# Kernel optimization log

Measured on AMD Instinct MI355X. Metric: run time of the kernel, lower is better.

Reference implementation:

```python
import jax, jax.numpy as jnp
import numpy as np

N, E, F_IN, H, C = 50000, 800000, 128, 4, 73
HC = H * C  # 292
NEG_SLOPE_ATT = 0.2   # GATv2 attention leaky relu
NEG_SLOPE_ACT = 0.01  # F.leaky_relu default
BN_EPS = 1e-5


def setup_inputs() -> dict:
    key = jax.random.key(0)
    ks = jax.random.split(key, 20)
    rn = lambda k, shp, s=0.05: (jax.random.normal(k, shp, jnp.float32) * s)
    inp = {
        'x': jax.random.normal(ks[0], (N, F_IN), jnp.float32),
        'edge_index': jax.random.randint(ks[1], (2, E), 0, N, jnp.int64),
        # conv1 (in=F_IN)
        'Wl1': rn(ks[2], (HC, F_IN)), 'bl1': rn(ks[3], (HC,)),
        'Wr1': rn(ks[4], (HC, F_IN)), 'br1': rn(ks[5], (HC,)),
        'att1': rn(ks[6], (H, C)), 'b1': rn(ks[7], (HC,)),
        # conv2 (in=HC)
        'Wl2': rn(ks[8], (HC, HC)), 'bl2': rn(ks[9], (HC,)),
        'Wr2': rn(ks[10], (HC, HC)), 'br2': rn(ks[11], (HC,)),
        'att2': rn(ks[12], (H, C)), 'b2': rn(ks[13], (HC,)),
        # shared BatchNorm1d(HC)
        'gamma': jnp.ones((HC,), jnp.float32), 'beta': jnp.zeros((HC,), jnp.float32),
        # classifier Linear(HC, 2)
        'Wc': rn(ks[14], (2, HC)), 'bc': rn(ks[15], (2,)),
    }
    return inp


def _gatv2(x, src, dst, Wl, bl, Wr, br, att, b):
    # lin_l on source, lin_r on target (PyG GATv2Conv, share_weights=False)
    xl = (x @ Wl.T + bl).reshape(-1, H, C)  # [N,H,C]
    xr = (x @ Wr.T + br).reshape(-1, H, C)
    f = xl[src] + xr[dst]                    # [E,H,C] edge-wise gather
    s = jnp.einsum('ehc,hc->eh', jax.nn.leaky_relu(f, NEG_SLOPE_ATT), att)
    # segment softmax over incoming edges of each destination node
    m = jax.ops.segment_max(s, dst, num_segments=N)
    ex = jnp.exp(s - m[dst])
    den = jax.ops.segment_sum(ex, dst, num_segments=N)
    alpha = ex / (den[dst] + 1e-16)          # [E,H]
    out = jax.ops.segment_sum(alpha[:, :, None] * xl[src], dst, num_segments=N)
    return out.reshape(-1, HC) + b           # concat heads + bias


def _bn(x, gamma, beta):
    mu = jnp.mean(x, axis=0)
    var = jnp.mean((x - mu) ** 2, axis=0)
    return (x - mu) * jax.lax.rsqrt(var + BN_EPS) * gamma + beta


def reference(x, edge_index, Wl1, bl1, Wr1, br1, att1, b1,
              Wl2, bl2, Wr2, br2, att2, b2, gamma, beta, Wc, bc):
    src, dst = edge_index[0], edge_index[1]
    h = _gatv2(x, src, dst, Wl1, bl1, Wr1, br1, att1, b1)
    h = jax.nn.leaky_relu(_bn(h, gamma, beta), NEG_SLOPE_ACT)
    h = _gatv2(h, src, dst, Wl2, bl2, Wr2, br2, att2, b2)
    h = jax.nn.leaky_relu(_bn(h, gamma, beta), NEG_SLOPE_ACT)
    return h @ Wc.T + bc
```

## Files before the change

### kernel.cpp

```cpp
#include <hip/hip_runtime.h>

#define HCDIM 292
#define NHEAD 4
#define CDIM 73
#define SLOTS 5
#define NPERM 320
#define BN_EPS 1e-5f

using u16x8 = __attribute__((ext_vector_type(8))) unsigned short;
using s16x8 = __attribute__((ext_vector_type(8))) short;
using f32x4 = __attribute__((ext_vector_type(4))) float;
using u16x4 = __attribute__((ext_vector_type(4))) unsigned short;

__device__ inline ushort f2bf(float f) {
  unsigned int u = __float_as_uint(f);
  u += 0x7FFFu + ((u >> 16) & 1u);
  return (ushort)(u >> 16);
}
__device__ inline float bf2f(ushort v) {
  return __uint_as_float(((unsigned int)v) << 16);
}

__device__ inline int perm2feat(int p, bool& valid) {
  int h, c;
  if (p < 256) {
    h = p >> 6;
    c = ((p & 3) << 4) | ((p >> 2) & 15);
    valid = true;
  } else {
    int q = p - 256;
    h = q >> 4;
    c = 64 + (q & 15);
    valid = (q & 15) < (CDIM - 64);
  }
  return h * CDIM + c;
}

__global__ void k_zero_i32(int* __restrict__ p, int n) {
  int i = blockIdx.x * blockDim.x + threadIdx.x;
  if (i < n) p[i] = 0;
}
__global__ void k_zero_f32(float* __restrict__ p, int n) {
  int i = blockIdx.x * blockDim.x + threadIdx.x;
  if (i < n) p[i] = 0.f;
}

__global__ void k_wperm(const float* __restrict__ W, const float* __restrict__ b,
                        ushort* __restrict__ Wp, float* __restrict__ pb,
                        int Kin, int Kpad, int kperm) {
  int p = blockIdx.x, t = threadIdx.x;
  bool pv;
  int gn = perm2feat(p, pv);
  int gk = t;
  bool kv = t < Kin;
  if (kperm) { bool v2; gk = perm2feat(t, v2); kv = v2; }
  ushort v = 0;
  if (pv && kv) v = f2bf(W[(size_t)gn * Kin + gk]);
  Wp[(size_t)p * Kpad + t] = v;
  if (t == 0) pb[p] = pv ? b[gn] : 0.f;
}

__global__ void k_vecperm(const float* __restrict__ att1, const float* __restrict__ b1,
                          const float* __restrict__ att2, const float* __restrict__ b2,
                          const float* __restrict__ gamma, const float* __restrict__ beta,
                          const float* __restrict__ Wc, float* __restrict__ o) {
  int p = threadIdx.x, w = blockIdx.x;
  bool pv;
  int gn = perm2feat(p, pv);
  const float* src;
  switch (w) {
    case 0: src = att1; break;
    case 1: src = b1; break;
    case 2: src = att2; break;
    case 3: src = b2; break;
    case 4: src = gamma; break;
    case 5: src = beta; break;
    case 6: src = Wc; break;
    default: src = Wc + HCDIM; break;
  }
  o[w * NPERM + p] = pv ? src[gn] : 0.f;
}

__global__ void k_hist(const int* __restrict__ dst, int* __restrict__ deg, int E) {
  int i = blockIdx.x * blockDim.x + threadIdx.x;
  if (i < E) atomicAdd(&deg[dst[i]], 1);
}

__global__ __launch_bounds__(256) void k_block_sum(const int* __restrict__ deg,
                                                   int* __restrict__ bsum, int n) {
  __shared__ int s[256];
  int i = blockIdx.x * 256 + threadIdx.x;
  s[threadIdx.x] = (i < n) ? deg[i] : 0;
  __syncthreads();
  for (int off = 128; off > 0; off >>= 1) {
    if (threadIdx.x < off) s[threadIdx.x] += s[threadIdx.x + off];
    __syncthreads();
  }
  if (threadIdx.x == 0) bsum[blockIdx.x] = s[0];
}

__global__ __launch_bounds__(256) void k_scan_small(const int* __restrict__ bsum,
                                                    int* __restrict__ boff, int G) {
  __shared__ int s[256];
  int t = threadIdx.x;
  int v = (t < G) ? bsum[t] : 0;
  s[t] = v;
  __syncthreads();
  for (int off = 1; off < 256; off <<= 1) {
    int tv = (t >= off) ? s[t - off] : 0;
    __syncthreads();
    s[t] += tv;
    __syncthreads();
  }
  if (t < G) boff[t] = s[t] - v;
}

__global__ __launch_bounds__(256) void k_scan_final(const int* __restrict__ deg,
                                                    const int* __restrict__ boff,
                                                    int* __restrict__ row_ptr,
                                                    int* __restrict__ cursor,
                                                    int n, int E) {
  __shared__ int s[256];
  int t = threadIdx.x;
  int i = blockIdx.x * 256 + t;
  int v = (i < n) ? deg[i] : 0;
  s[t] = v;
  __syncthreads();
  for (int off = 1; off < 256; off <<= 1) {
    int tv = (t >= off) ? s[t - off] : 0;
    __syncthreads();
    s[t] += tv;
    __syncthreads();
  }
  if (i < n) {
    int rp = boff[blockIdx.x] + s[t] - v;
    row_ptr[i] = rp;
    cursor[i] = rp;
  }
  if (i == 0) row_ptr[n] = E;
}

__global__ void k_csr_fill(const int* __restrict__ srcs, const int* __restrict__ dsts,
                           int* __restrict__ cursor, int* __restrict__ csr_src, int E) {
  int i = blockIdx.x * blockDim.x + threadIdx.x;
  if (i < E) {
    int pos = atomicAdd(&cursor[dsts[i]], 1);
    csr_src[pos] = srcs[i];
  }
}

template <bool CVT>
__device__ inline void load_frags(const char* const (&Ar)[4],
                                  const ushort* const (&Br)[5], int koff, int quad,
                                  s16x8 (&af)[4], s16x8 (&bf)[5]) {
#pragma unroll
  for (int i = 0; i < 4; ++i) {
    if (CVT) {
      const float* p = (const float*)Ar[i] + koff + quad * 8;
      float4 f0 = *(const float4*)p;
      float4 f1 = *(const float4*)(p + 4);
      s16x8 v;
      v[0] = (short)f2bf(f0.x); v[1] = (short)f2bf(f0.y);
      v[2] = (short)f2bf(f0.z); v[3] = (short)f2bf(f0.w);
      v[4] = (short)f2bf(f1.x); v[5] = (short)f2bf(f1.y);
      v[6] = (short)f2bf(f1.z); v[7] = (short)f2bf(f1.w);
      af[i] = v;
    } else {
      af[i] = *(const s16x8*)((const ushort*)Ar[i] + koff + quad * 8);
    }
  }
#pragma unroll
  for (int i = 0; i < 5; ++i)
    bf[i] = *(const s16x8*)(Br[i] + koff + quad * 8);
}

__device__ inline void mfma_block(const s16x8 (&af)[4], const s16x8 (&bf)[5],
                                  f32x4 (&acc)[4][5]) {
#pragma unroll
  for (int mi = 0; mi < 4; ++mi)
#pragma unroll
    for (int ni = 0; ni < 5; ++ni)
      acc[mi][ni] = __builtin_amdgcn_mfma_f32_16x16x32_bf16(bf[ni], af[mi],
                                                            acc[mi][ni], 0, 0, 0);
}

template <int KS, bool CVT>
__global__ __launch_bounds__(256) void k_gemm_direct(
    const void* __restrict__ Av, const ushort* __restrict__ Wb,
    const float* __restrict__ pb, ushort* __restrict__ o0,
    ushort* __restrict__ o1, int M, int mt) {
  int b = blockIdx.x;
  int x = b & 7, g = b >> 3;
  int ct = g & 3, mq = g >> 2;
  int m = mq * 8 + x;
  if (m >= mt) return;
  const int bm = m * 128;
  ushort* out = (ct < 2) ? o0 : o1;
  const int colbase = (ct & 1) * 160;
  const int wrow0 = ct * 160;
  const int tid = threadIdx.x;
  const int wave = tid >> 6, lane = tid & 63;
  const int quad = lane >> 4, lr = lane & 15;
  const int wm = (wave & 1) * 64, wn = (wave >> 1) * 80;

  f32x4 acc[4][5] = {};

  const char* Ar[4];
  const ushort* Br[5];
  const int esz = CVT ? 4 : 2;
#pragma unroll
  for (int i = 0; i < 4; ++i) {
    int ar = bm + wm + i * 16 + lr;
    if (ar >= M) ar = M - 1;
    Ar[i] = (const char*)Av + (size_t)ar * KS * esz;
  }
#pragma unroll
  for (int i = 0; i < 5; ++i)
    Br[i] = Wb + (size_t)(wrow0 + wn + i * 16 + lr) * KS;

  s16x8 afA[4], bfA[5], afB[4], bfB[5];
  load_frags<CVT>(Ar, Br, 0, quad, afA, bfA);
#pragma unroll
  for (int k0 = 0; k0 < KS; k0 += 64) {
    if (k0 + 32 < KS) load_frags<CVT>(Ar, Br, k0 + 32, quad, afB, bfB);
    mfma_block(afA, bfA, acc);
    if (k0 + 32 < KS) {
      if (k0 + 64 < KS) load_frags<CVT>(Ar, Br, k0 + 64, quad, afA, bfA);
      mfma_block(afB, bfB, acc);
    }
  }

#pragma unroll
  for (int mi = 0; mi < 4; ++mi) {
    int gm = bm + wm + mi * 16 + lr;
    if (gm >= M) continue;
    ushort* orow = out + (size_t)gm * NPERM + colbase + wn + quad * 4;
#pragma unroll
    for (int ni = 0; ni < 5; ++ni) {
      float4 pbv = *(const float4*)(pb + wrow0 + wn + ni * 16 + quad * 4);
      u16x4 o;
      o[0] = f2bf(acc[mi][ni][0] + pbv.x);
      o[1] = f2bf(acc[mi][ni][1] + pbv.y);
      o[2] = f2bf(acc[mi][ni][2] + pbv.z);
      o[3] = f2bf(acc[mi][ni][3] + pbv.w);
      *(u16x4*)(orow + ni * 16) = o;
    }
  }
}

__global__ __launch_bounds__(256) void k_pre(const ushort* __restrict__ xl,
                                             const float* __restrict__ attp,
                                             float* __restrict__ pl, int n) {
  int wave = threadIdx.x >> 6, lane = threadIdx.x & 63;
  int d = blockIdx.x * 4 + wave;
  if (d >= n) return;
  int hgrp = lane >> 4, li = lane & 15;
  u16x4 a4 = *(const u16x4*)(xl + (size_t)d * NPERM + lane * 4);
  ushort a1 = xl[(size_t)d * NPERM + 256 + lane];
  float Ta = 0.f;
#pragma unroll
  for (int k = 0; k < 4; ++k) Ta = fmaf(bf2f(a4[k]), attp[lane * 4 + k], Ta);
  Ta = fmaf(bf2f(a1), attp[256 + lane], Ta);
#pragma unroll
  for (int off = 1; off < 16; off <<= 1) Ta += __shfl_xor(Ta, off, 64);
  if (li == 0) pl[d * 4 + hgrp] = 0.6f * Ta;
}

__global__ __launch_bounds__(256) void k_agg(const ushort* __restrict__ xl,
                                             const ushort* __restrict__ xr,
                                             const float* __restrict__ pl,
                                             const int* __restrict__ csr_src,
                                             const int* __restrict__ row_ptr,
                                             const float* __restrict__ attp,
                                             const float* __restrict__ bp,
                                             ushort* __restrict__ out, int n) {
  int wave = threadIdx.x >> 6, lane = threadIdx.x & 63;
  int d = blockIdx.x * 4 + wave;
  if (d >= n) return;
  int hgrp = lane >> 4;
  int start = __builtin_amdgcn_readfirstlane(row_ptr[d]);
  int end = __builtin_amdgcn_readfirstlane(row_ptr[d + 1]);

  float bpv[SLOTS];
#pragma unroll
  for (int k = 0; k < 4; ++k) bpv[k] = bp[lane * 4 + k];
  bpv[4] = bp[256 + lane];

  if (start >= end) {
    u16x4 o4;
#pragma unroll
    for (int k = 0; k < 4; ++k) o4[k] = f2bf(bpv[k]);
    *(u16x4*)(out + (size_t)d * NPERM + lane * 4) = o4;
    out[(size_t)d * NPERM + 256 + lane] = f2bf(bpv[4]);
    return;
  }

  float xrv[SLOTS], attv[SLOTS], acc[SLOTS] = {};
  {
    u16x4 r4 = *(const u16x4*)(xr + (size_t)d * NPERM + lane * 4);
#pragma unroll
    for (int k = 0; k < 4; ++k) {
      xrv[k] = bf2f(r4[k]);
      attv[k] = 0.4f * attp[lane * 4 + k];
    }
    xrv[4] = bf2f(xr[(size_t)d * NPERM + 256 + lane]);
    attv[4] = 0.4f * attp[256 + lane];
  }
  float Tb = 0.f;
#pragma unroll
  for (int k = 0; k < SLOTS; ++k) Tb = fmaf(xrv[k], attv[k], Tb);
  Tb += __shfl_xor(Tb, 1, 64);
  Tb += __shfl_xor(Tb, 2, 64);
  Tb += __shfl_xor(Tb, 4, 64);
  Tb += __shfl_xor(Tb, 8, 64);
  float prv = 1.5f * Tb;
  float den = 0.f;
  int dg = end - start;

  int sA = __builtin_amdgcn_readfirstlane(csr_src[start]);
  int eB0 = (dg > 1) ? start + 1 : start;
  int sB = __builtin_amdgcn_readfirstlane(csr_src[eB0]);
  u16x4 a4 = *(const u16x4*)(xl + (size_t)sA * NPERM + lane * 4);
  ushort a1 = xl[(size_t)sA * NPERM + 256 + lane];
  float plA = pl[sA * 4 + hgrp];
  u16x4 b4 = *(const u16x4*)(xl + (size_t)sB * NPERM + lane * 4);
  ushort b1 = xl[(size_t)sB * NPERM + 256 + lane];
  float plB = pl[sB * 4 + hgrp];

  for (int e = start; e + 1 < end; e += 2) {
    int p0 = (e + 2 < end) ? e + 2 : end - 1;
    int p1 = (e + 3 < end) ? e + 3 : end - 1;
    int t0 = __builtin_amdgcn_readfirstlane(csr_src[p0]);
    int t1 = __builtin_amdgcn_readfirstlane(csr_src[p1]);
    u16x4 n4a = *(const u16x4*)(xl + (size_t)t0 * NPERM + lane * 4);
    ushort n1a = xl[(size_t)t0 * NPERM + 256 + lane];
    float plN0 = pl[t0 * 4 + hgrp];
    u16x4 n4b = *(const u16x4*)(xl + (size_t)t1 * NPERM + lane * 4);
    ushort n1b = xl[(size_t)t1 * NPERM + 256 + lane];
    float plN1 = pl[t1 * 4 + hgrp];

    float xa[SLOTS] = {bf2f(a4[0]), bf2f(a4[1]), bf2f(a4[2]), bf2f(a4[3]), bf2f(a1)};
    float xb[SLOTS] = {bf2f(b4[0]), bf2f(b4[1]), bf2f(b4[2]), bf2f(b4[3]), bf2f(b1)};
    float Ta = 0.f, Tc = 0.f;
#pragma unroll
    for (int k = 0; k < SLOTS; ++k) {
      Ta = fmaf(fabsf(xa[k] + xrv[k]), attv[k], Ta);
      Tc = fmaf(fabsf(xb[k] + xrv[k]), attv[k], Tc);
    }
    Ta += __shfl_xor(Ta, 1, 64);  Tc += __shfl_xor(Tc, 1, 64);
    Ta += __shfl_xor(Ta, 2, 64);  Tc += __shfl_xor(Tc, 2, 64);
    Ta += __shfl_xor(Ta, 4, 64);  Tc += __shfl_xor(Tc, 4, 64);
    Ta += __shfl_xor(Ta, 8, 64);  Tc += __shfl_xor(Tc, 8, 64);
    float sa_ = fminf(Ta + plA + prv, 60.f);
    float sb_ = fminf(Tc + plB + prv, 60.f);
    float wa = __expf(sa_);
    float wb = __expf(sb_);
    den += wa + wb;
#pragma unroll
    for (int k = 0; k < SLOTS; ++k) {
      acc[k] = fmaf(wa, xa[k], acc[k]);
      acc[k] = fmaf(wb, xb[k], acc[k]);
    }
    a4 = n4a; a1 = n1a; plA = plN0;
    b4 = n4b; b1 = n1b; plB = plN1;
  }

  if (dg & 1) {
    float xa[SLOTS] = {bf2f(a4[0]), bf2f(a4[1]), bf2f(a4[2]), bf2f(a4[3]), bf2f(a1)};
    float Ta = 0.f;
#pragma unroll
    for (int k = 0; k < SLOTS; ++k)
      Ta = fmaf(fabsf(xa[k] + xrv[k]), attv[k], Ta);
    Ta += __shfl_xor(Ta, 1, 64);
    Ta += __shfl_xor(Ta, 2, 64);
    Ta += __shfl_xor(Ta, 4, 64);
    Ta += __shfl_xor(Ta, 8, 64);
    float wa = __expf(fminf(Ta + plA + prv, 60.f));
    den += wa;
#pragma unroll
    for (int k = 0; k < SLOTS; ++k) acc[k] = fmaf(wa, xa[k], acc[k]);
  }

  float inv = 1.f / (den + 1e-16f);
  u16x4 o4;
#pragma unroll
  for (int k = 0; k < 4; ++k) o4[k] = f2bf(fmaf(acc[k], inv, bpv[k]));
  *(u16x4*)(out + (size_t)d * NPERM + lane * 4) = o4;
  out[(size_t)d * NPERM + 256 + lane] = f2bf(fmaf(acc[4], inv, bpv[4]));
}

__global__ __launch_bounds__(320) void k_bn_reduce(const ushort* __restrict__ h,
                                                   float* __restrict__ colsum,
                                                   float* __restrict__ colsq,
                                                   int n, int rows_per_block) {
  int c = threadIdx.x;
  int r0 = blockIdx.x * rows_per_block;
  int r1 = min(r0 + rows_per_block, n);
  float s = 0.f, s2 = 0.f;
  for (int r = r0; r < r1; ++r) {
    float v = bf2f(h[(size_t)r * NPERM + c]);
    s += v;
    s2 += v * v;
  }
  atomicAdd(&colsum[c], s);
  atomicAdd(&colsq[c], s2);
}

__global__ void k_bn_coef(float* __restrict__ colsum, float* __restrict__ colsq,
                          const float* __restrict__ gp, const float* __restrict__ bp,
                          float invN) {
  int c = threadIdx.x + blockIdx.x * blockDim.x;
  if (c >= NPERM) return;
  float mu = colsum[c] * invN;
  float var = colsq[c] * invN - mu * mu;
  float scale = rsqrtf(var + BN_EPS) * gp[c];
  colsum[c] = scale;
  colsq[c] = bp[c] - mu * scale;
}

__global__ void k_bn_apply_bf(const ushort* __restrict__ h,
                              const float* __restrict__ scale,
                              const float* __restrict__ shift,
                              ushort* __restrict__ outb, int total8) {
  int i = blockIdx.x * blockDim.x + threadIdx.x;
  if (i >= total8) return;
  int cg = i - (i / 40) * 40;
  u16x8 v = *(const u16x8*)(h + (size_t)i * 8);
  u16x8 o;
#pragma unroll
  for (int k = 0; k < 8; ++k) {
    int c = cg * 8 + k;
    float f = fmaf(bf2f(v[k]), scale[c], shift[c]);
    f = (f > 0.f) ? f : 0.01f * f;
    o[k] = f2bf(f);
  }
  *(u16x8*)(outb + (size_t)i * 8) = o;
}

__global__ __launch_bounds__(256) void k_bn_classifier(
    const ushort* __restrict__ h, const float* __restrict__ scale,
    const float* __restrict__ shift, const float* __restrict__ wc0,
    const float* __restrict__ wc1, const float* __restrict__ bc,
    float* __restrict__ out, int n) {
  int wave = threadIdx.x >> 6, lane = threadIdx.x & 63;
  int r = blockIdx.x * 4 + wave;
  if (r >= n) return;
  float a0 = 0.f, a1 = 0.f;
#pragma unroll
  for (int k = 0; k < SLOTS; ++k) {
    int slot = lane + 64 * k;
    float v = fmaf(bf2f(h[(size_t)r * NPERM + slot]), scale[slot], shift[slot]);
    v = (v > 0.f) ? v : 0.01f * v;
    a0 = fmaf(v, wc0[slot], a0);
    a1 = fmaf(v, wc1[slot], a1);
  }
#pragma unroll
  for (int off = 32; off > 0; off >>= 1) {
    a0 += __shfl_xor(a0, off, 64);
    a1 += __shfl_xor(a1, off, 64);
  }
  if (lane == 0) {
    out[(size_t)2 * r] = a0 + bc[0];
    out[(size_t)2 * r + 1] = a1 + bc[1];
  }
}

extern "C" void kernel_launch(void* const* d_in, const int* in_sizes, int n_in,
                              void* d_out, int out_size, void* d_ws, size_t ws_size,
                              hipStream_t stream) {
  const float* x      = (const float*)d_in[0];
  const int*   eidx   = (const int*)d_in[1];
  const float* Wl1    = (const float*)d_in[2];
  const float* bl1    = (const float*)d_in[3];
  const float* Wr1    = (const float*)d_in[4];
  const float* br1    = (const float*)d_in[5];
  const float* att1   = (const float*)d_in[6];
  const float* b1     = (const float*)d_in[7];
  const float* Wl2    = (const float*)d_in[8];
  const float* bl2    = (const float*)d_in[9];
  const float* Wr2    = (const float*)d_in[10];
  const float* br2    = (const float*)d_in[11];
  const float* att2   = (const float*)d_in[12];
  const float* b2     = (const float*)d_in[13];
  const float* gamma  = (const float*)d_in[14];
  const float* beta   = (const float*)d_in[15];
  const float* Wc     = (const float*)d_in[16];
  const float* bc     = (const float*)d_in[17];
  float* out = (float*)d_out;

  const int FIN = 128;
  const int N = in_sizes[0] / FIN;
  const int E = in_sizes[1] / 2;

  const int* src = eidx;
  const int* dst = eidx + E;

  ushort* h      = (ushort*)d_ws;
  ushort* xl     = h + (size_t)N * NPERM;
  ushort* xr     = xl + (size_t)N * NPERM;
  ushort* abuf   = xr + (size_t)N * NPERM;
  ushort* wb     = abuf + (size_t)N * NPERM;
  float* pb      = (float*)(wb + (size_t)2 * NPERM * NPERM);
  float* vecp    = pb + 2 * NPERM;
  float* pl      = vecp + 8 * NPERM;
  float* colsum  = pl + (size_t)N * NHEAD;
  float* colsq   = colsum + NPERM;
  int* deg       = (int*)(colsq + NPERM);
  int* row_ptr   = deg + N;
  int* cursor    = row_ptr + N + 1;
  int* bsum      = cursor + N;
  int* boff      = bsum + 256;
  int* csr_src   = boff + 256;

  const int G = (N + 255) / 256;
  const int EB = (E + 255) / 256;
  const int AGGB = (N + 3) / 4;
  const int mt = (N + 127) / 128;
  const int GEMMB = 8 * 4 * ((mt + 7) / 8);

  const float* att1p = vecp;
  const float* b1p   = vecp + NPERM;
  const float* att2p = vecp + 2 * NPERM;
  const float* b2p   = vecp + 3 * NPERM;
  const float* gp    = vecp + 4 * NPERM;
  const float* btp   = vecp + 5 * NPERM;
  const float* wc0   = vecp + 6 * NPERM;
  const float* wc1   = vecp + 7 * NPERM;

  k_zero_i32<<<G, 256, 0, stream>>>(deg, N);
  k_hist<<<EB, 256, 0, stream>>>(dst, deg, E);
  k_block_sum<<<G, 256, 0, stream>>>(deg, bsum, N);
  k_scan_small<<<1, 256, 0, stream>>>(bsum, boff, G);
  k_scan_final<<<G, 256, 0, stream>>>(deg, boff, row_ptr, cursor, N, E);
  k_csr_fill<<<EB, 256, 0, stream>>>(src, dst, cursor, csr_src, E);

  k_vecperm<<<8, NPERM, 0, stream>>>(att1, b1, att2, b2, gamma, beta, Wc, vecp);

  k_wperm<<<NPERM, FIN, 0, stream>>>(Wl1, bl1, wb, pb, FIN, FIN, 0);
  k_wperm<<<NPERM, FIN, 0, stream>>>(Wr1, br1, wb + (size_t)NPERM * FIN, pb + NPERM,
                                     FIN, FIN, 0);
  k_gemm_direct<FIN, true><<<GEMMB, 256, 0, stream>>>((const void*)x, wb, pb,
                                                      xl, xr, N, mt);
  k_pre<<<AGGB, 256, 0, stream>>>(xl, att1p, pl, N);
  k_agg<<<AGGB, 256, 0, stream>>>(xl, xr, pl, csr_src, row_ptr, att1p, b1p, h, N);

  const int RPB = (N + 255) / 256;
  k_zero_f32<<<1, 2 * NPERM, 0, stream>>>(colsum, 2 * NPERM);
  k_bn_reduce<<<256, NPERM, 0, stream>>>(h, colsum, colsq, N, RPB);
  k_bn_coef<<<2, 160, 0, stream>>>(colsum, colsq, gp, btp, 1.f / (float)N);
  k_bn_apply_bf<<<(N * 40 + 255) / 256, 256, 0, stream>>>(h, colsum, colsq, abuf,
                                                          N * 40);

  k_wperm<<<NPERM, NPERM, 0, stream>>>(Wl2, bl2, wb, pb, HCDIM, NPERM, 1);
  k_wperm<<<NPERM, NPERM, 0, stream>>>(Wr2, br2, wb + (size_t)NPERM * NPERM,
                                       pb + NPERM, HCDIM, NPERM, 1);
  k_gemm_direct<NPERM, false><<<GEMMB, 256, 0, stream>>>((const void*)abuf, wb, pb,
                                                         xl, xr, N, mt);
  k_pre<<<AGGB, 256, 0, stream>>>(xl, att2p, pl, N);
  k_agg<<<AGGB, 256, 0, stream>>>(xl, xr, pl, csr_src, row_ptr, att2p, b2p, h, N);

  k_zero_f32<<<1, 2 * NPERM, 0, stream>>>(colsum, 2 * NPERM);
  k_bn_reduce<<<256, NPERM, 0, stream>>>(h, colsum, colsq, N, RPB);
  k_bn_coef<<<2, 160, 0, stream>>>(colsum, colsq, gp, btp, 1.f / (float)N);

  k_bn_classifier<<<AGGB, 256, 0, stream>>>(h, colsum, colsq, wc0, wc1, bc, out, N);
}
```

Before: 657.4 us.

## Stage weight tiles in LDS and loop persistent GEMM blocks over row tiles

The GEMM becomes a persistent kernel of 512 blocks. Each block loads an 80-column weight slice into shared memory once, then walks row tiles of 256 with stride 64, reading B fragments from LDS instead of global memory. The A fragments are double-buffered across k-steps, and the bias values are hoisted out of the row loop. The small zeroing kernels are replaced with hipMemsetAsync. The risk is lower parallelism per block and LDS bank conflicts or occupancy limits from the padded weight tile.

```diff
diff --git a/kernel.cpp b/kernel.cpp
--- a/kernel.cpp
+++ b/kernel.cpp
@@ -34,15 +34,6 @@
     valid = (q & 15) < (CDIM - 64);
   }
   return h * CDIM + c;
-}
-
-__global__ void k_zero_i32(int* __restrict__ p, int n) {
-  int i = blockIdx.x * blockDim.x + threadIdx.x;
-  if (i < n) p[i] = 0;
-}
-__global__ void k_zero_f32(float* __restrict__ p, int n) {
-  int i = blockIdx.x * blockDim.x + threadIdx.x;
-  if (i < n) p[i] = 0.f;
 }
 
 __global__ void k_wperm(const float* __restrict__ W, const float* __restrict__ b,
@@ -150,9 +141,8 @@
 }
 
 template <bool CVT>
-__device__ inline void load_frags(const char* const (&Ar)[4],
-                                  const ushort* const (&Br)[5], int koff, int quad,
-                                  s16x8 (&af)[4], s16x8 (&bf)[5]) {
+__device__ inline void load_af(const char* const (&Ar)[4], int koff, int quad,
+                               s16x8 (&af)[4]) {
 #pragma unroll
   for (int i = 0; i < 4; ++i) {
     if (CVT) {
@@ -169,81 +159,82 @@
       af[i] = *(const s16x8*)((const ushort*)Ar[i] + koff + quad * 8);
     }
   }
-#pragma unroll
-  for (int i = 0; i < 5; ++i)
-    bf[i] = *(const s16x8*)(Br[i] + koff + quad * 8);
-}
-
-__device__ inline void mfma_block(const s16x8 (&af)[4], const s16x8 (&bf)[5],
-                                  f32x4 (&acc)[4][5]) {
-#pragma unroll
-  for (int mi = 0; mi < 4; ++mi)
-#pragma unroll
-    for (int ni = 0; ni < 5; ++ni)
-      acc[mi][ni] = __builtin_amdgcn_mfma_f32_16x16x32_bf16(bf[ni], af[mi],
-                                                            acc[mi][ni], 0, 0, 0);
 }
 
 template <int KS, bool CVT>
-__global__ __launch_bounds__(256) void k_gemm_direct(
+__global__ __launch_bounds__(256) void k_gemm_blds(
     const void* __restrict__ Av, const ushort* __restrict__ Wb,
     const float* __restrict__ pb, ushort* __restrict__ o0,
-    ushort* __restrict__ o1, int M, int mt) {
+    ushort* __restrict__ o1, int M, int miters) {
+  constexpr int KSTEPS = KS / 32;
+  constexpr int BSTR = KS + 8;
+  __shared__ ushort Bs[80 * BSTR];
   int b = blockIdx.x;
-  int x = b & 7, g = b >> 3;
-  int ct = g & 3, mq = g >> 2;
-  int m = mq * 8 + x;
-  if (m >= mt) return;
-  const int bm = m * 128;
-  ushort* out = (ct < 2) ? o0 : o1;
-  const int colbase = (ct & 1) * 160;
-  const int wrow0 = ct * 160;
+  int mlo = b & 7, ct = (b >> 3) & 7, mhi = b >> 6;
+  int mc = mlo + 8 * mhi;
+  ushort* out = (ct < 4) ? o0 : o1;
+  const int colbase = (ct & 3) * 80;
   const int tid = threadIdx.x;
   const int wave = tid >> 6, lane = tid & 63;
   const int quad = lane >> 4, lr = lane & 15;
-  const int wm = (wave & 1) * 64, wn = (wave >> 1) * 80;
-
-  f32x4 acc[4][5] = {};
-
-  const char* Ar[4];
-  const ushort* Br[5];
   const int esz = CVT ? 4 : 2;
-#pragma unroll
-  for (int i = 0; i < 4; ++i) {
-    int ar = bm + wm + i * 16 + lr;
-    if (ar >= M) ar = M - 1;
-    Ar[i] = (const char*)Av + (size_t)ar * KS * esz;
-  }
-#pragma unroll
-  for (int i = 0; i < 5; ++i)
-    Br[i] = Wb + (size_t)(wrow0 + wn + i * 16 + lr) * KS;
-
-  s16x8 afA[4], bfA[5], afB[4], bfB[5];
-  load_frags<CVT>(Ar, Br, 0, quad, afA, bfA);
-#pragma unroll
-  for (int k0 = 0; k0 < KS; k0 += 64) {
-    if (k0 + 32 < KS) load_frags<CVT>(Ar, Br, k0 + 32, quad, afB, bfB);
-    mfma_block(afA, bfA, acc);
-    if (k0 + 32 < KS) {
-      if (k0 + 64 < KS) load_frags<CVT>(Ar, Br, k0 + 64, quad, afA, bfA);
-      mfma_block(afB, bfB, acc);
-    }
-  }
-
-#pragma unroll
-  for (int mi = 0; mi < 4; ++mi) {
-    int gm = bm + wm + mi * 16 + lr;
-    if (gm >= M) continue;
-    ushort* orow = out + (size_t)gm * NPERM + colbase + wn + quad * 4;
-#pragma unroll
-    for (int ni = 0; ni < 5; ++ni) {
-      float4 pbv = *(const float4*)(pb + wrow0 + wn + ni * 16 + quad * 4);
-      u16x4 o;
-      o[0] = f2bf(acc[mi][ni][0] + pbv.x);
-      o[1] = f2bf(acc[mi][ni][1] + pbv.y);
-      o[2] = f2bf(acc[mi][ni][2] + pbv.z);
-      o[3] = f2bf(acc[mi][ni][3] + pbv.w);
-      *(u16x4*)(orow + ni * 16) = o;
+
+  for (int idx = tid; idx < 80 * (KS / 8); idx += 256) {
+    int r = idx / (KS / 8), c8 = idx - r * (KS / 8);
+    *(u16x8*)(Bs + r * BSTR + c8 * 8) =
+        *(const u16x8*)(Wb + (size_t)(ct * 80 + r) * KS + c8 * 8);
+  }
+  __syncthreads();
+
+  const ushort* bp[5];
+#pragma unroll
+  for (int i = 0; i < 5; ++i) bp[i] = Bs + (i * 16 + lr) * BSTR;
+
+  float4 pbv[5];
+#pragma unroll
+  for (int ni = 0; ni < 5; ++ni)
+    pbv[ni] = *(const float4*)(pb + ct * 80 + ni * 16 + quad * 4);
+
+  for (int it = mc; it < miters; it += 64) {
+    int mbase = it * 256 + wave * 64;
+    const char* Ar[4];
+#pragma unroll
+    for (int i = 0; i < 4; ++i) {
+      int ar = mbase + i * 16 + lr;
+      if (ar >= M) ar = M - 1;
+      Ar[i] = (const char*)Av + (size_t)ar * KS * esz;
+    }
+    f32x4 acc[4][5] = {};
+    s16x8 afb[2][4];
+    load_af<CVT>(Ar, 0, quad, afb[0]);
+#pragma unroll
+    for (int s = 0; s < KSTEPS; ++s) {
+      if (s + 1 < KSTEPS) load_af<CVT>(Ar, (s + 1) * 32, quad, afb[(s + 1) & 1]);
+      s16x8 bf[5];
+#pragma unroll
+      for (int i = 0; i < 5; ++i)
+        bf[i] = *(const s16x8*)(bp[i] + s * 32 + quad * 8);
+#pragma unroll
+      for (int ni = 0; ni < 5; ++ni)
+#pragma unroll
+        for (int mi = 0; mi < 4; ++mi)
+          acc[mi][ni] = __builtin_amdgcn_mfma_f32_16x16x32_bf16(
+              bf[ni], afb[s & 1][mi], acc[mi][ni], 0, 0, 0);
+    }
+#pragma unroll
+    for (int mi = 0; mi < 4; ++mi) {
+      int gm = mbase + mi * 16 + lr;
+      if (gm >= M) continue;
+      ushort* orow = out + (size_t)gm * NPERM + colbase + quad * 4;
+#pragma unroll
+      for (int ni = 0; ni < 5; ++ni) {
+        u16x4 o;
+        o[0] = f2bf(acc[mi][ni][0] + pbv[ni].x);
+        o[1] = f2bf(acc[mi][ni][1] + pbv[ni].y);
+        o[2] = f2bf(acc[mi][ni][2] + pbv[ni].z);
+        o[3] = f2bf(acc[mi][ni][3] + pbv[ni].w);
+        *(u16x4*)(orow + ni * 16) = o;
+      }
     }
   }
 }
@@ -515,8 +506,8 @@
   const int G = (N + 255) / 256;
   const int EB = (E + 255) / 256;
   const int AGGB = (N + 3) / 4;
-  const int mt = (N + 127) / 128;
-  const int GEMMB = 8 * 4 * ((mt + 7) / 8);
+  const int MITERS = (N + 255) / 256;
+  const int GEMMB = 512;
 
   const float* att1p = vecp;
   const float* b1p   = vecp + NPERM;
@@ -527,7 +518,7 @@
   const float* wc0   = vecp + 6 * NPERM;
   const float* wc1   = vecp + 7 * NPERM;
 
-  k_zero_i32<<<G, 256, 0, stream>>>(deg, N);
+  hipMemsetAsync(deg, 0, (size_t)N * sizeof(int), stream);
   k_hist<<<EB, 256, 0, stream>>>(dst, deg, E);
   k_block_sum<<<G, 256, 0, stream>>>(deg, bsum, N);
   k_scan_small<<<1, 256, 0, stream>>>(bsum, boff, G);
@@ -539,13 +530,13 @@
   k_wperm<<<NPERM, FIN, 0, stream>>>(Wl1, bl1, wb, pb, FIN, FIN, 0);
   k_wperm<<<NPERM, FIN, 0, stream>>>(Wr1, br1, wb + (size_t)NPERM * FIN, pb + NPERM,
                                      FIN, FIN, 0);
-  k_gemm_direct<FIN, true><<<GEMMB, 256, 0, stream>>>((const void*)x, wb, pb,
-                                                      xl, xr, N, mt);
+  k_gemm_blds<FIN, true><<<GEMMB, 256, 0, stream>>>((const void*)x, wb, pb,
+                                                    xl, xr, N, MITERS);
   k_pre<<<AGGB, 256, 0, stream>>>(xl, att1p, pl, N);
   k_agg<<<AGGB, 256, 0, stream>>>(xl, xr, pl, csr_src, row_ptr, att1p, b1p, h, N);
 
   const int RPB = (N + 255) / 256;
-  k_zero_f32<<<1, 2 * NPERM, 0, stream>>>(colsum, 2 * NPERM);
+  hipMemsetAsync(colsum, 0, 2 * NPERM * sizeof(float), stream);
   k_bn_reduce<<<256, NPERM, 0, stream>>>(h, colsum, colsq, N, RPB);
   k_bn_coef<<<2, 160, 0, stream>>>(colsum, colsq, gp, btp, 1.f / (float)N);
   k_bn_apply_bf<<<(N * 40 + 255) / 256, 256, 0, stream>>>(h, colsum, colsq, abuf,
@@ -554,12 +545,12 @@
   k_wperm<<<NPERM, NPERM, 0, stream>>>(Wl2, bl2, wb, pb, HCDIM, NPERM, 1);
   k_wperm<<<NPERM, NPERM, 0, stream>>>(Wr2, br2, wb + (size_t)NPERM * NPERM,
                                        pb + NPERM, HCDIM, NPERM, 1);
-  k_gemm_direct<NPERM, false><<<GEMMB, 256, 0, stream>>>((const void*)abuf, wb, pb,
-                                                         xl, xr, N, mt);
+  k_gemm_blds<NPERM, false><<<GEMMB, 256, 0, stream>>>((const void*)abuf, wb, pb,
+                                                       xl, xr, N, MITERS);
   k_pre<<<AGGB, 256, 0, stream>>>(xl, att2p, pl, N);
   k_agg<<<AGGB, 256, 0, stream>>>(xl, xr, pl, csr_src, row_ptr, att2p, b2p, h, N);
 
-  k_zero_f32<<<1, 2 * NPERM, 0, stream>>>(colsum, 2 * NPERM);
+  hipMemsetAsync(colsum, 0, 2 * NPERM * sizeof(float), stream);
   k_bn_reduce<<<256, NPERM, 0, stream>>>(h, colsum, colsq, N, RPB);
   k_bn_coef<<<2, 160, 0, stream>>>(colsum, colsq, gp, btp, 1.f / (float)N);
 
```

Result: faster. 635.2 us (-3.4%).
